# Kernel tuning notes

Measured on AMD Instinct MI355X. Metric: run time of the kernel, lower is better.

The kernel has to match this reference:

```python
import jax, jax.numpy as jnp
import numpy as np

S, B, D, H, FF, L, V, O = 512, 32, 512, 8, 2048, 6, 32000, 1000
DH = D // H
EPS = 1e-5


def layer_norm(x, g, b):
    mu = jnp.mean(x, axis=-1, keepdims=True)
    var = jnp.mean((x - mu) ** 2, axis=-1, keepdims=True)
    return (x - mu) * jax.lax.rsqrt(var + EPS) * g + b


def positional_encoding(seq_len, dim):
    pos = np.arange(seq_len, dtype=np.float32)[:, None]
    i = np.arange(dim)
    angle = pos / (10000.0 ** ((i // 2 * 2.0) / dim))
    pe = np.where(i % 2 == 0, np.sin(angle), np.cos(angle)).astype(np.float32)
    return jnp.asarray(pe)  # [seq_len, dim]


def setup_inputs() -> dict:
    key = jax.random.key(0)
    ks = jax.random.split(key, 16)
    sc = 0.02
    inp = {
        'x': jax.random.randint(ks[0], (S, B), 0, V, dtype=jnp.int32),
        'x_len': jnp.full((B,), S, dtype=jnp.int32),
        'emb': jax.random.normal(ks[1], (V, D), jnp.float32) * sc,
        'Wq': jax.random.normal(ks[2], (L, D, D), jnp.float32) * sc,
        'bq': jnp.zeros((L, D), jnp.float32),
        'Wk': jax.random.normal(ks[3], (L, D, D), jnp.float32) * sc,
        'bk': jnp.zeros((L, D), jnp.float32),
        'Wv': jax.random.normal(ks[4], (L, D, D), jnp.float32) * sc,
        'bv': jnp.zeros((L, D), jnp.float32),
        'Wo': jax.random.normal(ks[5], (L, D, D), jnp.float32) * sc,
        'bo': jnp.zeros((L, D), jnp.float32),
        'ln1_g': jnp.ones((L, D), jnp.float32),
        'ln1_b': jnp.zeros((L, D), jnp.float32),
        'W1': jax.random.normal(ks[6], (L, D, FF), jnp.float32) * sc,
        'b1': jnp.zeros((L, FF), jnp.float32),
        'W2': jax.random.normal(ks[7], (L, FF, D), jnp.float32) * sc,
        'b2': jnp.zeros((L, D), jnp.float32),
        'ln2_g': jnp.ones((L, D), jnp.float32),
        'ln2_b': jnp.zeros((L, D), jnp.float32),
        'W_fc': jax.random.normal(ks[8], (S * D, O), jnp.float32) * sc,
        'b_fc': jnp.zeros((O,), jnp.float32),
    }
    return inp


def reference(x, x_len, emb, Wq, bq, Wk, bk, Wv, bv, Wo, bo, ln1_g, ln1_b,
              W1, b1, W2, b2, ln2_g, ln2_b, W_fc, b_fc):
    out = emb[x]                      # [S, B, D]
    out = jnp.transpose(out, (1, 0, 2))  # [B, S, D]
    out = out + positional_encoding(S, D)[None, :, :]
    scale = DH ** -0.5
    for l in range(L):
        # NOTE: faithful to the original buggy head-split: plain row-major
        # reshape [B,S,D] -> [B*H,S,DH] without a [B,H,S,DH] transpose.
        q = jnp.reshape(out @ Wq[l] + bq[l], (B * H, S, DH))
        k = jnp.reshape(out @ Wk[l] + bk[l], (B * H, S, DH))
        v = jnp.reshape(out @ Wv[l] + bv[l], (B * H, S, DH))
        attn = jax.nn.softmax(jnp.einsum('gqd,gkd->gqk', q, k) * scale, axis=-1)
        ctx = jnp.einsum('gqk,gkd->gqd', attn, v).reshape(B, S, D)
        h = layer_norm(ctx @ Wo[l] + bo[l] + out, ln1_g[l], ln1_b[l])
        f = jax.nn.relu(h @ W1[l] + b1[l]) @ W2[l] + b2[l]
        out = layer_norm(f + h, ln2_g[l], ln2_b[l])
    out = out.reshape(B, S * D)
    return out @ W_fc + b_fc          # [B, O]
```

## Files before the change

kernel.cpp:

```cpp
#include <hip/hip_runtime.h>
#include <cstdint>
#include <cstddef>

#define S_  512
#define B_  32
#define D_  512
#define FF_ 2048
#define L_  6
#define O_  1000
#define M_  (B_*S_)
#define G_  256
#define DH_ 64

typedef __attribute__((ext_vector_type(8))) short bf16x8;
typedef __attribute__((ext_vector_type(4))) float f32x4;
typedef __attribute__((ext_vector_type(16))) float f32x16;

__device__ __forceinline__ unsigned short f2bf(float f) {
  unsigned int u = __builtin_bit_cast(unsigned int, f);
  u = (u + 0x7fffu + ((u >> 16) & 1u)) >> 16;
  return (unsigned short)u;
}
__device__ __forceinline__ float bf2f(unsigned short u) {
  return __builtin_bit_cast(float, (unsigned int)u << 16);
}
__device__ __forceinline__ unsigned int pkbf(float a, float b) {
  return (unsigned int)f2bf(a) | ((unsigned int)f2bf(b) << 16);
}
__device__ __forceinline__ unsigned int prm(float a, float b) {
  return __builtin_amdgcn_perm(__builtin_bit_cast(unsigned int, b),
                               __builtin_bit_cast(unsigned int, a), 0x07060302u);
}
__device__ __forceinline__ void gload_lds16(const void* g, void* l) {
  __builtin_amdgcn_global_load_lds(
      (const __attribute__((address_space(1))) unsigned int*)g,
      (__attribute__((address_space(3))) unsigned int*)l, 16, 0, 0);
}

__global__ void pe_kernel(float* __restrict__ pe) {
  int i = blockIdx.x * 256 + threadIdx.x;
  int s = i >> 9, d = i & 511;
  double de = (double)(d & ~1);
  double ang = (double)s * exp(de * (-9.210340371976184 / 512.0));
  pe[i] = (d & 1) ? (float)cos(ang) : (float)sin(ang);
}

__global__ void wconv_kernel(const float* __restrict__ W, unsigned short* __restrict__ Wt,
                             int K, int N, size_t ozs) {
  __shared__ float tile[32][33];
  const float* Wl = W + (size_t)blockIdx.z * K * N;
  unsigned short* Wtl = Wt + (size_t)blockIdx.z * ozs;
  int k0 = blockIdx.x * 32, n0 = blockIdx.y * 32;
  int c = threadIdx.x & 31, rb = threadIdx.x >> 5;
#pragma unroll
  for (int i = 0; i < 4; ++i) {
    int r = rb + i * 8;
    tile[r][c] = Wl[(size_t)(k0 + r) * N + n0 + c];
  }
  __syncthreads();
#pragma unroll
  for (int i = 0; i < 4; ++i) {
    int r = rb + i * 8;
    Wtl[(size_t)(n0 + r) * K + k0 + c] = f2bf(tile[c][r]);
  }
}

__global__ void embed_kernel(const int* __restrict__ x, const float* __restrict__ emb,
                             const float* __restrict__ pe, unsigned short* __restrict__ xb) {
  int bi = blockIdx.x;
  int s = bi / B_, b = bi % B_;
  int tok = x[s * B_ + b];
  int d = threadIdx.x * 4;
  float4 e = *(const float4*)(emb + (size_t)tok * D_ + d);
  float4 p = *(const float4*)(pe + (size_t)s * D_ + d);
  size_t o = ((size_t)b * S_ + s) * D_ + d;
  ushort4 u;
  u.x = f2bf(e.x + p.x); u.y = f2bf(e.y + p.y);
  u.z = f2bf(e.z + p.z); u.w = f2bf(e.w + p.w);
  *(ushort4*)(xb + o) = u;
}

__global__ __launch_bounds__(256, 3) void gemm128_kernel(
    const unsigned short* __restrict__ A, const unsigned short* __restrict__ Bt,
    const float* __restrict__ b0, const float* __restrict__ b1, const float* __restrict__ b2,
    unsigned short* __restrict__ o0, unsigned short* __restrict__ o1, unsigned short* __restrict__ o2,
    int K, int N, int relu, int split, int nbx) {
  __shared__ unsigned short As[2][128 * 32];
  __shared__ unsigned short Bs[2][128 * 32];
  int nwg = nbx * (M_ / 128);
  int cpx = nwg >> 3;
  int id = blockIdx.x;
  int wg = (id & 7) * cpx + (id >> 3);
  int bx = wg % nbx, by = wg / nbx;
  int m0 = by * 128, n0 = bx * 128;

  int tid = threadIdx.x, lane = tid & 63, wid = tid >> 6;
  int wm = wid >> 1, wn = wid & 1;
  f32x4 acc[4][4];
#pragma unroll
  for (int mi = 0; mi < 4; ++mi)
#pragma unroll
    for (int ni = 0; ni < 4; ++ni) acc[mi][ni] = (f32x4)0.0f;

  int srow = lane >> 2, scol = (lane & 3) * 8;
  const unsigned short* Abase = A + (size_t)m0 * K;
  const unsigned short* Bbase = Bt + (size_t)n0 * K;
  int c16 = lane & 15, hi = lane >> 4;
  int koff = hi * 8;
  int arow = wm * 64 + c16, brow = wn * 64 + c16;
  int nk = K >> 5;

  auto STAGE = [&](int kt, int bb) {
    int k0 = kt * 32;
#pragma unroll
    for (int i = 0; i < 2; ++i) {
      int c = wid * 2 + i;
      gload_lds16(Abase + (size_t)(c * 16 + srow) * K + k0 + scol, (char*)As[bb] + c * 1024);
      gload_lds16(Bbase + (size_t)(c * 16 + srow) * K + k0 + scol, (char*)Bs[bb] + c * 1024);
    }
  };

  STAGE(0, 0); STAGE(1, 1);
  int bb = 0;
  for (int kt = 0; kt < nk; ++kt) {
    if (kt + 1 < nk) asm volatile("s_waitcnt vmcnt(4)" ::: "memory");
    else             asm volatile("s_waitcnt vmcnt(0)" ::: "memory");
    __builtin_amdgcn_s_barrier();
    __builtin_amdgcn_sched_barrier(0);
    bf16x8 af[4], bfr[4];
#pragma unroll
    for (int mi = 0; mi < 4; ++mi) af[mi] = *(const bf16x8*)&As[bb][(arow + mi * 16) * 32 + koff];
#pragma unroll
    for (int ni = 0; ni < 4; ++ni) bfr[ni] = *(const bf16x8*)&Bs[bb][(brow + ni * 16) * 32 + koff];
    __builtin_amdgcn_s_setprio(1);
#pragma unroll
    for (int mi = 0; mi < 4; ++mi)
#pragma unroll
      for (int ni = 0; ni < 4; ++ni)
        acc[mi][ni] = __builtin_amdgcn_mfma_f32_16x16x32_bf16(bfr[ni], af[mi], acc[mi][ni], 0, 0, 0);
    __builtin_amdgcn_s_setprio(0);
    __builtin_amdgcn_sched_barrier(0);
    __builtin_amdgcn_s_barrier();
    if (kt + 2 < nk) STAGE(kt + 2, bb);
    bb ^= 1;
  }

  const float* bias = b0;
  unsigned short* outb = o0;
  int nbase = n0, ostride = N;
  if (split) {
    int seg = n0 >> 9;
    if (seg == 1) { bias = b1; outb = o1; }
    else if (seg == 2) { bias = b2; outb = o2; }
    nbase = n0 & 511; ostride = 512;
  }
#pragma unroll
  for (int ni = 0; ni < 4; ++ni) {
    int colb = nbase + wn * 64 + ni * 16 + hi * 4;
    float4 bv = *(const float4*)(bias + colb);
#pragma unroll
    for (int mi = 0; mi < 4; ++mi) {
      int row = m0 + wm * 64 + mi * 16 + c16;
      float v0 = acc[mi][ni][0] + bv.x;
      float v1 = acc[mi][ni][1] + bv.y;
      float v2 = acc[mi][ni][2] + bv.z;
      float v3 = acc[mi][ni][3] + bv.w;
      if (relu) { v0 = fmaxf(v0, 0.f); v1 = fmaxf(v1, 0.f); v2 = fmaxf(v2, 0.f); v3 = fmaxf(v3, 0.f); }
      *(uint2*)(outb + (size_t)row * ostride + colb) = make_uint2(pkbf(v0, v1), pkbf(v2, v3));
    }
  }
}

__global__ __launch_bounds__(256) void addln_kernel(
    const unsigned short* __restrict__ Y, const unsigned short* __restrict__ R,
    const float* __restrict__ g, const float* __restrict__ b,
    unsigned short* __restrict__ Out) {
  __shared__ float red[2][2], red2[2][2];
  int t = threadIdx.x;
  int rg = t >> 7;
  int tt = t & 127;
  int row = blockIdx.x * 2 + rg;
  size_t o = (size_t)row * 512 + tt * 4;
  ushort4 yv = *(const ushort4*)(Y + o);
  ushort4 rv = *(const ushort4*)(R + o);
  float v0 = bf2f(yv.x) + bf2f(rv.x);
  float v1 = bf2f(yv.y) + bf2f(rv.y);
  float v2 = bf2f(yv.z) + bf2f(rv.z);
  float v3 = bf2f(yv.w) + bf2f(rv.w);
  float s = v0 + v1 + v2 + v3;
#pragma unroll
  for (int m = 1; m < 64; m <<= 1) s += __shfl_xor(s, m);
  if ((tt & 63) == 0) red[rg][tt >> 6] = s;
  __syncthreads();
  float mean = (red[rg][0] + red[rg][1]) * (1.0f / 512.0f);
  float d0 = v0 - mean, d1 = v1 - mean, d2 = v2 - mean, d3 = v3 - mean;
  float sq = d0 * d0 + d1 * d1 + d2 * d2 + d3 * d3;
#pragma unroll
  for (int m = 1; m < 64; m <<= 1) sq += __shfl_xor(sq, m);
  if ((tt & 63) == 0) red2[rg][tt >> 6] = sq;
  __syncthreads();
  float var = (red2[rg][0] + red2[rg][1]) * (1.0f / 512.0f);
  float rstd = rsqrtf(var + 1e-5f);
  float4 gg = *(const float4*)(g + tt * 4);
  float4 bb = *(const float4*)(b + tt * 4);
  float y0 = d0 * rstd * gg.x + bb.x;
  float y1 = d1 * rstd * gg.y + bb.y;
  float y2 = d2 * rstd * gg.z + bb.z;
  float y3 = d3 * rstd * gg.w + bb.w;
  *(uint2*)(Out + o) = make_uint2(pkbf(y0, y1), pkbf(y2, y3));
}

__global__ __launch_bounds__(256) void attn_kernel(
    const unsigned short* __restrict__ Q, const unsigned short* __restrict__ Kb,
    const unsigned short* __restrict__ Vb, unsigned short* __restrict__ Ctx) {
  __shared__ char KlB[2][8192];
  __shared__ char VtB[2][8192];
  int g = blockIdx.y;
  int q0 = blockIdx.x * 256;
  const unsigned short* Kg = Kb + (size_t)g * 512 * 64;
  const unsigned short* Vg = Vb + (size_t)g * 512 * 64;
  int tid = threadIdx.x, lane = tid & 63, wid = tid >> 6;
  int l31 = lane & 31, h = lane >> 5;
  bool lo = (lane < 32);
  int qrowA = q0 + wid * 64 + l31;
  int qrowB = qrowA + 32;
  const float sc2 = 0.125f * 1.44269504f;

  bf16x8 qfa[4], qfb[4];
  {
    const unsigned short* qpa = Q + ((size_t)g * 512 + qrowA) * 64;
    const unsigned short* qpb = Q + ((size_t)g * 512 + qrowB) * 64;
#pragma unroll
    for (int c = 0; c < 4; ++c) {
      bf16x8 ra = *(const bf16x8*)(qpa + c * 16 + h * 8);
      bf16x8 rb = *(const bf16x8*)(qpb + c * 16 + h * 8);
      union { unsigned int u[4]; bf16x8 v; } ua, ub;
#pragma unroll
      for (int j = 0; j < 4; ++j) {
        ua.u[j] = pkbf(bf2f((unsigned short)ra[2 * j]) * sc2,
                       bf2f((unsigned short)ra[2 * j + 1]) * sc2);
        ub.u[j] = pkbf(bf2f((unsigned short)rb[2 * j]) * sc2,
                       bf2f((unsigned short)rb[2 * j + 1]) * sc2);
      }
      qfa[c] = ua.v; qfb[c] = ub.v;
    }
  }

  f32x16 cA0 = (f32x16)0.0f, cA1 = (f32x16)0.0f;
  f32x16 cB0 = (f32x16)0.0f, cB1 = (f32x16)0.0f;
  float mrA = -3.0e38f, lsA = 0.0f;
  float mrB = -3.0e38f, lsB = 0.0f;

  int rowS = tid >> 2;
  int cbA = (tid & 3) * 16;
  int cbB = cbA + 64;
  int swA = cbA ^ ((rowS & 7) << 4);
  int swB = cbB ^ ((rowS & 7) << 4);

  bf16x8 kc0 = *(const bf16x8*)(Kg + (size_t)rowS * 64 + cbA / 2);
  bf16x8 kc1 = *(const bf16x8*)(Kg + (size_t)rowS * 64 + cbB / 2);
  bf16x8 vc0 = *(const bf16x8*)(Vg + (size_t)rowS * 64 + cbA / 2);
  bf16x8 vc1 = *(const bf16x8*)(Vg + (size_t)rowS * 64 + cbB / 2);

  int cur = 0;
  for (int kt = 0; kt < 8; ++kt) {
    char* Kl = KlB[cur];
    char* Vt = VtB[cur];
    *(bf16x8*)(Kl + rowS * 128 + swA) = kc0;
    *(bf16x8*)(Kl + rowS * 128 + swB) = kc1;
#pragma unroll
    for (int j = 0; j < 8; ++j) {
      int dA = cbA / 2 + j;
      int dB = cbB / 2 + j;
      *(unsigned short*)(Vt + dA * 128 + ((2 * rowS) ^ ((dA & 7) << 4))) = (unsigned short)vc0[j];
      *(unsigned short*)(Vt + dB * 128 + ((2 * rowS) ^ ((dB & 7) << 4))) = (unsigned short)vc1[j];
    }
    bf16x8 kn0, kn1, vn0, vn1;
    if (kt < 7) {
      size_t nb = (size_t)((kt + 1) * 64 + rowS) * 64;
      kn0 = *(const bf16x8*)(Kg + nb + cbA / 2);
      kn1 = *(const bf16x8*)(Kg + nb + cbB / 2);
      vn0 = *(const bf16x8*)(Vg + nb + cbA / 2);
      vn1 = *(const bf16x8*)(Vg + nb + cbB / 2);
    }
    __syncthreads();

#pragma unroll
    for (int sub = 0; sub < 2; ++sub) {
      f32x16 s0 = (f32x16)0.0f, s1 = (f32x16)0.0f;
#pragma unroll
      for (int c = 0; c < 4; ++c) {
        int cb = 32 * c + 16 * h;
        int sw = cb ^ ((l31 & 7) << 4);
        bf16x8 k0 = *(const bf16x8*)(Kl + l31 * 128 + sw);
        bf16x8 k1 = *(const bf16x8*)(Kl + (32 + l31) * 128 + sw);
        bf16x8 qf = sub ? qfb[c] : qfa[c];
        s0 = __builtin_amdgcn_mfma_f32_32x32x16_bf16(k0, qf, s0, 0, 0, 0);
        s1 = __builtin_amdgcn_mfma_f32_32x32x16_bf16(k1, qf, s1, 0, 0, 0);
      }

      float mr = sub ? mrB : mrA;
      float ls = sub ? lsB : lsA;
      float pm = s0[0];
#pragma unroll
      for (int i = 1; i < 16; ++i) pm = fmaxf(pm, s0[i]);
#pragma unroll
      for (int i = 0; i < 16; ++i) pm = fmaxf(pm, s1[i]);
      pm = fmaxf(pm, __shfl_xor(pm, 32));
      if (!__all(pm <= mr + 8.0f)) {
        float mnew = fmaxf(mr, pm);
        float alpha = exp2f(mr - mnew);
        ls *= alpha;
        if (sub) {
#pragma unroll
          for (int i = 0; i < 16; ++i) { cB0[i] *= alpha; cB1[i] *= alpha; }
        } else {
#pragma unroll
          for (int i = 0; i < 16; ++i) { cA0[i] *= alpha; cA1[i] *= alpha; }
        }
        mr = mnew;
      }
      float p[32];
      float rs = 0.0f;
#pragma unroll
      for (int i = 0; i < 16; ++i) { p[i] = exp2f(s0[i] - mr); rs += p[i]; }
#pragma unroll
      for (int i = 0; i < 16; ++i) { p[16 + i] = exp2f(s1[i] - mr); rs += p[16 + i]; }
      float rso = __shfl_xor(rs, 32);
      ls += rs + rso;
      if (sub) { mrB = mr; lsB = ls; } else { mrA = mr; lsA = ls; }

      union { unsigned int u[4]; bf16x8 v; } pa[4];
#pragma unroll
      for (int t = 0; t < 2; ++t) {
#pragma unroll
        for (int u = 0; u < 2; ++u) {
#pragma unroll
          for (int pr = 0; pr < 2; ++pr) {
            const int b0i = t * 16 + 8 * u;
            unsigned int a  = prm(p[b0i + 2 * pr],     p[b0i + 2 * pr + 1]);
            unsigned int b  = prm(p[b0i + 4 + 2 * pr], p[b0i + 4 + 2 * pr + 1]);
            unsigned int sa = __shfl_xor(a, 32);
            unsigned int sb = __shfl_xor(b, 32);
            pa[t * 2 + u].u[pr]     = lo ? a  : sb;
            pa[t * 2 + u].u[2 + pr] = lo ? sa : b;
          }
        }
      }

#pragma unroll
      for (int kc = 0; kc < 4; ++kc) {
        int cb = 32 * kc + 16 * h;
        int sw = cb ^ ((l31 & 7) << 4);
        bf16x8 v0 = *(const bf16x8*)(Vt + l31 * 128 + sw);
        bf16x8 v1 = *(const bf16x8*)(Vt + (32 + l31) * 128 + sw);
        if (sub) {
          cB0 = __builtin_amdgcn_mfma_f32_32x32x16_bf16(v0, pa[kc].v, cB0, 0, 0, 0);
          cB1 = __builtin_amdgcn_mfma_f32_32x32x16_bf16(v1, pa[kc].v, cB1, 0, 0, 0);
        } else {
          cA0 = __builtin_amdgcn_mfma_f32_32x32x16_bf16(v0, pa[kc].v, cA0, 0, 0, 0);
          cA1 = __builtin_amdgcn_mfma_f32_32x32x16_bf16(v1, pa[kc].v, cA1, 0, 0, 0);
        }
      }
    }

    if (kt < 7) { kc0 = kn0; kc1 = kn1; vc0 = vn0; vc1 = vn1; }
    cur ^= 1;
  }

#pragma unroll
  for (int sub = 0; sub < 2; ++sub) {
    float inv = 1.0f / (sub ? lsB : lsA);
    int qrow = sub ? qrowB : qrowA;
    unsigned short* cp = Ctx + ((size_t)g * 512 + qrow) * 64;
#pragma unroll
    for (int dh = 0; dh < 2; ++dh) {
#pragma unroll
      for (int rq = 0; rq < 4; ++rq) {
        float e0 = (sub ? (dh ? cB1[rq * 4 + 0] : cB0[rq * 4 + 0]) : (dh ? cA1[rq * 4 + 0] : cA0[rq * 4 + 0])) * inv;
        float e1 = (sub ? (dh ? cB1[rq * 4 + 1] : cB0[rq * 4 + 1]) : (dh ? cA1[rq * 4 + 1] : cA0[rq * 4 + 1])) * inv;
        float e2 = (sub ? (dh ? cB1[rq * 4 + 2] : cB0[rq * 4 + 2]) : (dh ? cA1[rq * 4 + 2] : cA0[rq * 4 + 2])) * inv;
        float e3 = (sub ? (dh ? cB1[rq * 4 + 3] : cB0[rq * 4 + 3]) : (dh ? cA1[rq * 4 + 3] : cA0[rq * 4 + 3])) * inv;
        int d0 = dh * 32 + rq * 8 + h * 4;
        *(uint2*)(cp + d0) = make_uint2(pkbf(e0, e1), pkbf(e2, e3));
      }
    }
  }
}

#define KCH 1024
__global__ __launch_bounds__(512) void fc_part_kernel(const unsigned short* __restrict__ act,
                                                      const float* __restrict__ Wfc,
                                                      float* __restrict__ part) {
  __shared__ float al[32][256];
  int t = threadIdx.x;
  int kc = blockIdx.x;
  size_t k0 = (size_t)kc * KCH;
  int o1 = t;
  int o2 = 512 + t;
  bool a2 = (o2 < O_);
  float acc1[32], acc2[32];
#pragma unroll
  for (int bb = 0; bb < 32; ++bb) { acc1[bb] = 0.0f; acc2[bb] = 0.0f; }
  for (int sub = 0; sub < KCH / 256; ++sub) {
    __syncthreads();
    for (int i = t; i < 32 * 128; i += 512) {
      int bb = i >> 7, kk = (i & 127) * 2;
      ushort2 u = *(const ushort2*)(act + (size_t)bb * 262144 + k0 + sub * 256 + kk);
      al[bb][kk] = bf2f(u.x);
      al[bb][kk + 1] = bf2f(u.y);
    }
    __syncthreads();
    const float* wp = Wfc + (k0 + sub * 256) * O_;
    for (int kk = 0; kk < 256; kk += 4) {
      const float* wr = wp + (size_t)kk * O_;
      float w10 = wr[o1];
      float w11 = wr[O_ + o1];
      float w12 = wr[2 * O_ + o1];
      float w13 = wr[3 * O_ + o1];
      float w20 = a2 ? wr[o2] : 0.0f;
      float w21 = a2 ? wr[O_ + o2] : 0.0f;
      float w22 = a2 ? wr[2 * O_ + o2] : 0.0f;
      float w23 = a2 ? wr[3 * O_ + o2] : 0.0f;
#pragma unroll
      for (int bb = 0; bb < 32; ++bb) {
        f32x4 av = *(const f32x4*)&al[bb][kk];
        acc1[bb] = fmaf(av[0], w10, acc1[bb]);
        acc1[bb] = fmaf(av[1], w11, acc1[bb]);
        acc1[bb] = fmaf(av[2], w12, acc1[bb]);
        acc1[bb] = fmaf(av[3], w13, acc1[bb]);
        acc2[bb] = fmaf(av[0], w20, acc2[bb]);
        acc2[bb] = fmaf(av[1], w21, acc2[bb]);
        acc2[bb] = fmaf(av[2], w22, acc2[bb]);
        acc2[bb] = fmaf(av[3], w23, acc2[bb]);
      }
    }
  }
#pragma unroll
  for (int bb = 0; bb < 32; ++bb) {
    part[((size_t)kc * 32 + bb) * O_ + o1] = acc1[bb];
    if (a2) part[((size_t)kc * 32 + bb) * O_ + o2] = acc2[bb];
  }
}

__global__ void fc_reduce_kernel(const float* __restrict__ part, const float* __restrict__ bfc,
                                 float* __restrict__ out) {
  int o = blockIdx.x * 256 + threadIdx.x;
  int b = blockIdx.y;
  if (o >= O_) return;
  float s = bfc[o];
  for (int c = 0; c < 256; ++c) s += part[((size_t)c * 32 + b) * O_ + o];
  out[(size_t)b * O_ + o] = s;
}

extern "C" void kernel_launch(void* const* d_in, const int* in_sizes, int n_in,
                              void* d_out, int out_size, void* d_ws, size_t ws_size,
                              hipStream_t stream) {
  const int*   x   = (const int*)d_in[0];
  const float* emb = (const float*)d_in[2];
  const float* Wq  = (const float*)d_in[3];
  const float* bq  = (const float*)d_in[4];
  const float* Wk  = (const float*)d_in[5];
  const float* bk  = (const float*)d_in[6];
  const float* Wv  = (const float*)d_in[7];
  const float* bv  = (const float*)d_in[8];
  const float* Wo  = (const float*)d_in[9];
  const float* bo  = (const float*)d_in[10];
  const float* g1  = (const float*)d_in[11];
  const float* bn1 = (const float*)d_in[12];
  const float* W1  = (const float*)d_in[13];
  const float* bf1 = (const float*)d_in[14];
  const float* W2  = (const float*)d_in[15];
  const float* bf2 = (const float*)d_in[16];
  const float* g2  = (const float*)d_in[17];
  const float* bn2 = (const float*)d_in[18];
  const float* Wfc = (const float*)d_in[19];
  const float* bfc = (const float*)d_in[20];
  float* out = (float*)d_out;

  char* ws = (char*)d_ws;
  size_t off = 0;
  auto take = [&](size_t bytes) { char* p = ws + off; off += (bytes + 255) & ~(size_t)255; return p; };
  float*          pe   = (float*)take((size_t)512 * 512 * 4);
  unsigned short* wqkv = (unsigned short*)take((size_t)L_ * 1536 * 512 * 2);
  unsigned short* wot  = (unsigned short*)take((size_t)L_ * 512 * 512 * 2);
  unsigned short* w1t  = (unsigned short*)take((size_t)L_ * 2048 * 512 * 2);
  unsigned short* w2t  = (unsigned short*)take((size_t)L_ * 512 * 2048 * 2);
  unsigned short* xb   = (unsigned short*)take((size_t)M_ * 512 * 2);
  unsigned short* qb   = (unsigned short*)take((size_t)M_ * 512 * 2);
  unsigned short* kb   = (unsigned short*)take((size_t)M_ * 512 * 2);
  unsigned short* vb   = (unsigned short*)take((size_t)M_ * 512 * 2);
  unsigned short* cxb  = (unsigned short*)take((size_t)M_ * 512 * 2);
  unsigned short* hb   = (unsigned short*)take((size_t)M_ * 512 * 2);
  unsigned short* t1   = (unsigned short*)take((size_t)M_ * 512 * 2);
  unsigned short* f1b  = qb;
  float*          part = (float*)qb;

  pe_kernel<<<1024, 256, 0, stream>>>(pe);
  wconv_kernel<<<dim3(16, 16, L_), 256, 0, stream>>>(Wq, wqkv,          512, 512,  (size_t)1536 * 512);
  wconv_kernel<<<dim3(16, 16, L_), 256, 0, stream>>>(Wk, wqkv + 262144, 512, 512,  (size_t)1536 * 512);
  wconv_kernel<<<dim3(16, 16, L_), 256, 0, stream>>>(Wv, wqkv + 524288, 512, 512,  (size_t)1536 * 512);
  wconv_kernel<<<dim3(16, 16, L_), 256, 0, stream>>>(Wo, wot,           512, 512,  (size_t)512 * 512);
  wconv_kernel<<<dim3(16, 64, L_), 256, 0, stream>>>(W1, w1t,           512, 2048, (size_t)2048 * 512);
  wconv_kernel<<<dim3(64, 16, L_), 256, 0, stream>>>(W2, w2t,           2048, 512, (size_t)512 * 2048);
  embed_kernel<<<M_, 128, 0, stream>>>(x, emb, pe, xb);

  for (int l = 0; l < L_; ++l) {
    gemm128_kernel<<<1536, 256, 0, stream>>>(
        xb, wqkv + (size_t)l * 1536 * 512,
        bq + l * 512, bk + l * 512, bv + l * 512,
        qb, kb, vb, 512, 1536, 0, 1, 12);
    attn_kernel<<<dim3(2, G_), 256, 0, stream>>>(qb, kb, vb, cxb);
    gemm128_kernel<<<512, 256, 0, stream>>>(
        cxb, wot + (size_t)l * 512 * 512,
        bo + l * 512, nullptr, nullptr,
        t1, nullptr, nullptr, 512, 512, 0, 0, 4);
    addln_kernel<<<M_ / 2, 256, 0, stream>>>(t1, xb, g1 + l * 512, bn1 + l * 512, hb);
    gemm128_kernel<<<2048, 256, 0, stream>>>(
        hb, w1t + (size_t)l * 2048 * 512,
        bf1 + l * 2048, nullptr, nullptr,
        f1b, nullptr, nullptr, 512, 2048, 1, 0, 16);
    gemm128_kernel<<<512, 256, 0, stream>>>(
        f1b, w2t + (size_t)l * 512 * 2048,
        bf2 + l * 512, nullptr, nullptr,
        t1, nullptr, nullptr, 2048, 512, 0, 0, 4);
    addln_kernel<<<M_ / 2, 256, 0, stream>>>(t1, hb, g2 + l * 512, bn2 + l * 512, xb);
  }

  fc_part_kernel<<<256, 512, 0, stream>>>(xb, Wfc, part);
  fc_reduce_kernel<<<dim3(4, 32), 256, 0, stream>>>(part, bfc, out);
}
```

Before: 1.856 ms.

## Triple-buffer GEMM loads, one-wave-per-row LayerNorm, halve FC split chunk

The GEMM k-loop moves from double to triple buffering, staging three k-tiles ahead with adjusted vmcnt waits to hide more global-load latency. This raises LDS use per block, which may limit occupancy under launch_bounds(256,3). The add+LayerNorm kernel now handles one row per wavefront with 8 elements per lane, removing LDS reductions and __syncthreads. The FC split-K chunk is halved to launch twice as many blocks, at the cost of a longer reduction loop over partial sums.

```diff
diff --git a/kernel.cpp b/kernel.cpp
--- a/kernel.cpp
+++ b/kernel.cpp
@@ -85,8 +85,8 @@
     const float* __restrict__ b0, const float* __restrict__ b1, const float* __restrict__ b2,
     unsigned short* __restrict__ o0, unsigned short* __restrict__ o1, unsigned short* __restrict__ o2,
     int K, int N, int relu, int split, int nbx) {
-  __shared__ unsigned short As[2][128 * 32];
-  __shared__ unsigned short Bs[2][128 * 32];
+  __shared__ unsigned short As[3][128 * 32];
+  __shared__ unsigned short Bs[3][128 * 32];
   int nwg = nbx * (M_ / 128);
   int cpx = nwg >> 3;
   int id = blockIdx.x;
@@ -120,11 +120,13 @@
     }
   };
 
-  STAGE(0, 0); STAGE(1, 1);
+  STAGE(0, 0); STAGE(1, 1); STAGE(2, 2);
   int bb = 0;
   for (int kt = 0; kt < nk; ++kt) {
-    if (kt + 1 < nk) asm volatile("s_waitcnt vmcnt(4)" ::: "memory");
-    else             asm volatile("s_waitcnt vmcnt(0)" ::: "memory");
+    int rem = nk - 1 - kt;
+    if (rem >= 2)      asm volatile("s_waitcnt vmcnt(8)" ::: "memory");
+    else if (rem == 1) asm volatile("s_waitcnt vmcnt(4)" ::: "memory");
+    else               asm volatile("s_waitcnt vmcnt(0)" ::: "memory");
     __builtin_amdgcn_s_barrier();
     __builtin_amdgcn_sched_barrier(0);
     bf16x8 af[4], bfr[4];
@@ -141,8 +143,8 @@
     __builtin_amdgcn_s_setprio(0);
     __builtin_amdgcn_sched_barrier(0);
     __builtin_amdgcn_s_barrier();
-    if (kt + 2 < nk) STAGE(kt + 2, bb);
-    bb ^= 1;
+    if (kt + 3 < nk) STAGE(kt + 3, bb);
+    bb = (bb == 2) ? 0 : bb + 1;
   }
 
   const float* bias = b0;
@@ -175,39 +177,43 @@
     const unsigned short* __restrict__ Y, const unsigned short* __restrict__ R,
     const float* __restrict__ g, const float* __restrict__ b,
     unsigned short* __restrict__ Out) {
-  __shared__ float red[2][2], red2[2][2];
-  int t = threadIdx.x;
-  int rg = t >> 7;
-  int tt = t & 127;
-  int row = blockIdx.x * 2 + rg;
-  size_t o = (size_t)row * 512 + tt * 4;
-  ushort4 yv = *(const ushort4*)(Y + o);
-  ushort4 rv = *(const ushort4*)(R + o);
-  float v0 = bf2f(yv.x) + bf2f(rv.x);
-  float v1 = bf2f(yv.y) + bf2f(rv.y);
-  float v2 = bf2f(yv.z) + bf2f(rv.z);
-  float v3 = bf2f(yv.w) + bf2f(rv.w);
-  float s = v0 + v1 + v2 + v3;
+  int lane = threadIdx.x & 63, w = threadIdx.x >> 6;
+  int row = blockIdx.x * 4 + w;
+  size_t o = (size_t)row * 512 + lane * 8;
+  bf16x8 yv = *(const bf16x8*)(Y + o);
+  bf16x8 rv = *(const bf16x8*)(R + o);
+  float v[8];
+#pragma unroll
+  for (int j = 0; j < 8; ++j)
+    v[j] = bf2f((unsigned short)yv[j]) + bf2f((unsigned short)rv[j]);
+  float s = 0.0f;
+#pragma unroll
+  for (int j = 0; j < 8; ++j) s += v[j];
 #pragma unroll
   for (int m = 1; m < 64; m <<= 1) s += __shfl_xor(s, m);
-  if ((tt & 63) == 0) red[rg][tt >> 6] = s;
-  __syncthreads();
-  float mean = (red[rg][0] + red[rg][1]) * (1.0f / 512.0f);
-  float d0 = v0 - mean, d1 = v1 - mean, d2 = v2 - mean, d3 = v3 - mean;
-  float sq = d0 * d0 + d1 * d1 + d2 * d2 + d3 * d3;
+  float mean = s * (1.0f / 512.0f);
+  float sq = 0.0f;
+#pragma unroll
+  for (int j = 0; j < 8; ++j) { float d = v[j] - mean; sq += d * d; }
 #pragma unroll
   for (int m = 1; m < 64; m <<= 1) sq += __shfl_xor(sq, m);
-  if ((tt & 63) == 0) red2[rg][tt >> 6] = sq;
-  __syncthreads();
-  float var = (red2[rg][0] + red2[rg][1]) * (1.0f / 512.0f);
-  float rstd = rsqrtf(var + 1e-5f);
-  float4 gg = *(const float4*)(g + tt * 4);
-  float4 bb = *(const float4*)(b + tt * 4);
-  float y0 = d0 * rstd * gg.x + bb.x;
-  float y1 = d1 * rstd * gg.y + bb.y;
-  float y2 = d2 * rstd * gg.z + bb.z;
-  float y3 = d3 * rstd * gg.w + bb.w;
-  *(uint2*)(Out + o) = make_uint2(pkbf(y0, y1), pkbf(y2, y3));
+  float rstd = rsqrtf(sq * (1.0f / 512.0f) + 1e-5f);
+  float4 g0 = *(const float4*)(g + lane * 8);
+  float4 g1 = *(const float4*)(g + lane * 8 + 4);
+  float4 b0 = *(const float4*)(b + lane * 8);
+  float4 b1 = *(const float4*)(b + lane * 8 + 4);
+  float y0 = (v[0] - mean) * rstd * g0.x + b0.x;
+  float y1 = (v[1] - mean) * rstd * g0.y + b0.y;
+  float y2 = (v[2] - mean) * rstd * g0.z + b0.z;
+  float y3 = (v[3] - mean) * rstd * g0.w + b0.w;
+  float y4 = (v[4] - mean) * rstd * g1.x + b1.x;
+  float y5 = (v[5] - mean) * rstd * g1.y + b1.y;
+  float y6 = (v[6] - mean) * rstd * g1.z + b1.z;
+  float y7 = (v[7] - mean) * rstd * g1.w + b1.w;
+  uint4 u;
+  u.x = pkbf(y0, y1); u.y = pkbf(y2, y3);
+  u.z = pkbf(y4, y5); u.w = pkbf(y6, y7);
+  *(uint4*)(Out + o) = u;
 }
 
 __global__ __launch_bounds__(256) void attn_kernel(
@@ -388,7 +394,7 @@
   }
 }
 
-#define KCH 1024
+#define KCH 512
 __global__ __launch_bounds__(512) void fc_part_kernel(const unsigned short* __restrict__ act,
                                                       const float* __restrict__ Wfc,
                                                       float* __restrict__ part) {
@@ -449,7 +455,7 @@
   int b = blockIdx.y;
   if (o >= O_) return;
   float s = bfc[o];
-  for (int c = 0; c < 256; ++c) s += part[((size_t)c * 32 + b) * O_ + o];
+  for (int c = 0; c < 512; ++c) s += part[((size_t)c * 32 + b) * O_ + o];
   out[(size_t)b * O_ + o] = s;
 }
 
@@ -515,7 +521,7 @@
         cxb, wot + (size_t)l * 512 * 512,
         bo + l * 512, nullptr, nullptr,
         t1, nullptr, nullptr, 512, 512, 0, 0, 4);
-    addln_kernel<<<M_ / 2, 256, 0, stream>>>(t1, xb, g1 + l * 512, bn1 + l * 512, hb);
+    addln_kernel<<<M_ / 4, 256, 0, stream>>>(t1, xb, g1 + l * 512, bn1 + l * 512, hb);
     gemm128_kernel<<<2048, 256, 0, stream>>>(
         hb, w1t + (size_t)l * 2048 * 512,
         bf1 + l * 2048, nullptr, nullptr,
@@ -524,9 +530,9 @@
         f1b, w2t + (size_t)l * 512 * 2048,
         bf2 + l * 512, nullptr, nullptr,
         t1, nullptr, nullptr, 2048, 512, 0, 0, 4);
-    addln_kernel<<<M_ / 2, 256, 0, stream>>>(t1, hb, g2 + l * 512, bn2 + l * 512, xb);
-  }
-
-  fc_part_kernel<<<256, 512, 0, stream>>>(xb, Wfc, part);
+    addln_kernel<<<M_ / 4, 256, 0, stream>>>(t1, hb, g2 + l * 512, bn2 + l * 512, xb);
+  }
+
+  fc_part_kernel<<<512, 512, 0, stream>>>(xb, Wfc, part);
   fc_reduce_kernel<<<dim3(4, 32), 256, 0, stream>>>(part, bfc, out);
 }
```

Measured after the change: 1.775 ms (median of 2 runs). -4.4%, faster.
